# Kernel tuning notes

Hardware: AMD Instinct MI355X
Metric: run time of the kernel (lower is better)

The kernel has to match this reference:

```python
import jax, jax.numpy as jnp
import numpy as np

DIM = 1024
N_HEADS = 16
HEAD_DIM = DIM // N_HEADS


def setup_inputs() -> dict:
    key = jax.random.key(0)
    k_x, k_wqkv, k_bqkv, k_wp, k_bp = jax.random.split(key, 5)
    s = 1.0 / np.sqrt(DIM)
    return {
        "x": jax.random.normal(k_x, (2, 2048, DIM), dtype=jnp.float32),
        "w_qkv": jax.random.uniform(k_wqkv, (3 * DIM, DIM), minval=-s, maxval=s, dtype=jnp.float32),
        "b_qkv": jax.random.uniform(k_bqkv, (3 * DIM,), minval=-s, maxval=s, dtype=jnp.float32),
        "w_proj": jax.random.uniform(k_wp, (DIM, DIM), minval=-s, maxval=s, dtype=jnp.float32),
        "b_proj": jax.random.uniform(k_bp, (DIM,), minval=-s, maxval=s, dtype=jnp.float32),
    }


def reference(x, w_qkv, b_qkv, w_proj, b_proj):
    B, S, D = x.shape
    H, Hd = N_HEADS, HEAD_DIM
    scale = jnp.asarray(Hd, x.dtype) ** 0.5
    qkv = x @ w_qkv.T + b_qkv                      # [B, S, 3D]
    q, k, v = jnp.split(qkv, 3, axis=-1)
    # [B, S, D] -> [B, H, S, Hd]
    q = q.reshape(B, S, H, Hd).transpose(0, 2, 1, 3)
    k = k.reshape(B, S, H, Hd).transpose(0, 2, 1, 3)
    v = v.reshape(B, S, H, Hd).transpose(0, 2, 1, 3)
    attn = jnp.einsum("bhqd,bhkd->bhqk", q, k) / scale
    attn = jax.nn.softmax(attn, axis=-1)
    out = jnp.einsum("bhqk,bhkd->bhqd", attn, v)   # [B, H, S, Hd]
    out = out.transpose(0, 2, 1, 3).reshape(B, S, D)
    return out @ w_proj.T + b_proj
```

## Files before the change

kernel.cpp:

```cpp
#include <hip/hip_runtime.h>

typedef __bf16 bf16;
typedef __bf16 bf16x4 __attribute__((ext_vector_type(4)));
typedef __bf16 bf16x8 __attribute__((ext_vector_type(8)));
typedef float f32x4 __attribute__((ext_vector_type(4)));
typedef float f32x16 __attribute__((ext_vector_type(16)));

#define DIMD 1024
#define NHEAD 16
#define HDIM 64
#define BATCH 2
#define SEQ 2048
#define MTOT (BATCH*SEQ)

#define EXP2F(x) __builtin_amdgcn_exp2f(x)

#define OFF_VT (0ull)
#define OFF_OB (8ull<<20)

__device__ __forceinline__ bf16x8 cvt8(float4 a, float4 b) {
  bf16x8 r = { (bf16)a.x, (bf16)a.y, (bf16)a.z, (bf16)a.w,
               (bf16)b.x, (bf16)b.y, (bf16)b.z, (bf16)b.w };
  return r;
}

__global__ __launch_bounds__(256, 3) void gemm_qkv(
    const float* __restrict__ x, const float* __restrict__ W,
    const float* __restrict__ bias,
    bf16* __restrict__ Qb, bf16* __restrict__ Kb, bf16* __restrict__ Vt)
{
  __shared__ bf16 lA[2][128 * 32];
  __shared__ bf16 lB[2][128 * 32];
  const int tid = threadIdx.x;
  const int wave = tid >> 6, lane = tid & 63;
  const int l15 = lane & 15, quad = lane >> 4;
  const int wm = wave >> 1, wn = wave & 1;
  const int tm = blockIdx.y * 128, tn = blockIdx.x * 128;

  f32x4 acc[4][4] = {};

  const int srow = tid >> 1, shalf = (tid & 1) * 16;
  const float* ga = &x[(size_t)(tm + srow) * DIMD + shalf];
  const float* gb = &W[(size_t)(tn + srow) * DIMD + shalf];

  float4 av0 = ((const float4*)ga)[0], av1 = ((const float4*)ga)[1];
  float4 av2 = ((const float4*)ga)[2], av3 = ((const float4*)ga)[3];
  float4 bv0 = ((const float4*)gb)[0], bv1 = ((const float4*)gb)[1];
  float4 bv2 = ((const float4*)gb)[2], bv3 = ((const float4*)gb)[3];

  for (int kt = 0; kt < 32; kt++) {
    bf16* sA = lA[kt & 1];
    bf16* sB = lB[kt & 1];
    *(bf16x8*)&sA[srow * 32 + shalf]     = cvt8(av0, av1);
    *(bf16x8*)&sA[srow * 32 + shalf + 8] = cvt8(av2, av3);
    *(bf16x8*)&sB[srow * 32 + shalf]     = cvt8(bv0, bv1);
    *(bf16x8*)&sB[srow * 32 + shalf + 8] = cvt8(bv2, bv3);
    __syncthreads();

    const int kn = ((kt + 1) & 31) * 32;
    const float4* gan = (const float4*)(ga + kn);
    const float4* gbn = (const float4*)(gb + kn);
    av0 = gan[0]; av1 = gan[1]; av2 = gan[2]; av3 = gan[3];
    bv0 = gbn[0]; bv1 = gbn[1]; bv2 = gbn[2]; bv3 = gbn[3];

    bf16x8 af[4], bfr[4];
#pragma unroll
    for (int i = 0; i < 4; i++)
      af[i] = *(const bf16x8*)&sA[(wm * 64 + i * 16 + l15) * 32 + quad * 8];
#pragma unroll
    for (int i = 0; i < 4; i++)
      bfr[i] = *(const bf16x8*)&sB[(wn * 64 + i * 16 + l15) * 32 + quad * 8];
#pragma unroll
    for (int i = 0; i < 4; i++)
#pragma unroll
      for (int j = 0; j < 4; j++)
        acc[i][j] = __builtin_amdgcn_mfma_f32_16x16x32_bf16(af[i], bfr[j], acc[i][j], 0, 0, 0);
  }

  const int sel = tn >> 10;
#pragma unroll
  for (int j = 0; j < 4; j++) {
    const int n = tn + wn * 64 + j * 16 + l15;
    const float bv = bias[n];
    const int d = n & 1023, h = d >> 6, hd = d & 63;
#pragma unroll
    for (int i = 0; i < 4; i++) {
      const int mbase = tm + wm * 64 + i * 16 + quad * 4;
      const int b = mbase >> 11, s0 = mbase & 2047;
      const int bh = b * NHEAD + h;
      if (sel == 2) {
        bf16x4 vv = { (bf16)(acc[i][j][0] + bv), (bf16)(acc[i][j][1] + bv),
                      (bf16)(acc[i][j][2] + bv), (bf16)(acc[i][j][3] + bv) };
        *(bf16x4*)&Vt[((size_t)bh * HDIM + hd) * SEQ + s0] = vv;
      } else {
#pragma unroll
        for (int r = 0; r < 4; r++) {
          float v = acc[i][j][r] + bv;
          if (sel == 0)
            Qb[((size_t)bh * SEQ + s0 + r) * HDIM + hd] = (bf16)(v * 0.18033688f);
          else
            Kb[((size_t)bh * SEQ + s0 + r) * HDIM + hd] = (bf16)v;
        }
      }
    }
  }
}

__global__ __launch_bounds__(256, 2) void gemm_proj(
    const bf16* __restrict__ A, const float* __restrict__ W,
    const float* __restrict__ bias, float* __restrict__ out)
{
  __shared__ bf16 lA[2][64 * 32];
  __shared__ bf16 lB[2][128 * 32];
  const int tid = threadIdx.x;
  const int wave = tid >> 6, lane = tid & 63;
  const int l15 = lane & 15, quad = lane >> 4;
  const int tm = blockIdx.y * 64, tn = blockIdx.x * 128;

  f32x4 acc[4][2] = {};

  const int arow = tid >> 2, ach = (tid & 3) * 8;
  const int brow = tid >> 1, bhalf = (tid & 1) * 16;
  const bf16* ga = &A[(size_t)(tm + arow) * DIMD + ach];
  const float* gb = &W[(size_t)(tn + brow) * DIMD + bhalf];

  uint4 ar = *(const uint4*)ga;
  float4 bv0 = ((const float4*)gb)[0], bv1 = ((const float4*)gb)[1];
  float4 bv2 = ((const float4*)gb)[2], bv3 = ((const float4*)gb)[3];

  for (int kt = 0; kt < 32; kt++) {
    bf16* sA = lA[kt & 1];
    bf16* sB = lB[kt & 1];
    *(uint4*)&sA[arow * 32 + ach]        = ar;
    *(bf16x8*)&sB[brow * 32 + bhalf]     = cvt8(bv0, bv1);
    *(bf16x8*)&sB[brow * 32 + bhalf + 8] = cvt8(bv2, bv3);
    __syncthreads();

    const int kn = ((kt + 1) & 31) * 32;
    ar = *(const uint4*)(ga + kn);
    const float4* gbn = (const float4*)(gb + kn);
    bv0 = gbn[0]; bv1 = gbn[1]; bv2 = gbn[2]; bv3 = gbn[3];

    bf16x8 af[4], bfr[2];
#pragma unroll
    for (int i = 0; i < 4; i++)
      af[i] = *(const bf16x8*)&sA[(i * 16 + l15) * 32 + quad * 8];
#pragma unroll
    for (int j = 0; j < 2; j++)
      bfr[j] = *(const bf16x8*)&sB[(wave * 32 + j * 16 + l15) * 32 + quad * 8];
#pragma unroll
    for (int i = 0; i < 4; i++)
#pragma unroll
      for (int j = 0; j < 2; j++)
        acc[i][j] = __builtin_amdgcn_mfma_f32_16x16x32_bf16(af[i], bfr[j], acc[i][j], 0, 0, 0);
  }

#pragma unroll
  for (int j = 0; j < 2; j++) {
    const int n = tn + wave * 32 + j * 16 + l15;
    const float bv = bias[n];
#pragma unroll
    for (int i = 0; i < 4; i++) {
      const int mbase = tm + i * 16 + quad * 4;
#pragma unroll
      for (int r = 0; r < 4; r++)
        out[(size_t)(mbase + r) * DIMD + n] = acc[i][j][r] + bv;
    }
  }
}

#define LSTR 72
__global__ __launch_bounds__(256, 2) void attn_kernel(
    const bf16* __restrict__ Qb, const bf16* __restrict__ Kb,
    const bf16* __restrict__ Vt, bf16* __restrict__ Ob)
{
  __shared__ bf16 lKV[2][2][64 * LSTR];
  __shared__ bf16 lP[4][32 * LSTR];

  const int tid = threadIdx.x;
  const int wave = tid >> 6, lane = tid & 63;
  const int l31 = lane & 31, h = lane >> 5;
  const int xcd = blockIdx.x & 7, grp = blockIdx.x >> 3;
  const int bh = xcd + 8 * (grp & 3);
  const int qt = grp >> 2;

  const int qrow = qt * 128 + wave * 32 + l31;
  const bf16* qp = Qb + ((size_t)bh * SEQ + qrow) * HDIM + h * 8;
  bf16x8 qf[4];
#pragma unroll
  for (int c = 0; c < 4; c++) qf[c] = *(const bf16x8*)(qp + c * 16);

  const int srow = tid >> 3;
  const int sch = (tid & 7) * 8;
  const bf16* kg = Kb + ((size_t)bh * SEQ + srow) * HDIM + sch;
  const bf16* vg = Vt + ((size_t)bh * HDIM + srow) * SEQ + sch;

  uint4 kr0 = *(const uint4*)(kg);
  uint4 kr1 = *(const uint4*)(kg + 32 * HDIM);
  uint4 vr0 = *(const uint4*)(vg);
  uint4 vr1 = *(const uint4*)(vg + 32 * SEQ);

  f32x16 o0 = {}, o1 = {};
  float mrow = -1e30f, lrow = 0.f;

  for (int kt = 0; kt < SEQ / 64; kt++) {
    bf16* sK = lKV[kt & 1][0];
    bf16* sV = lKV[kt & 1][1];
    *(uint4*)&sK[srow * LSTR + sch]        = kr0;
    *(uint4*)&sK[(32 + srow) * LSTR + sch] = kr1;
    *(uint4*)&sV[srow * LSTR + sch]        = vr0;
    *(uint4*)&sV[(32 + srow) * LSTR + sch] = vr1;
    __syncthreads();

    const int ktn = (kt + 1) & (SEQ / 64 - 1);
    kr0 = *(const uint4*)(kg + (size_t)ktn * 64 * HDIM);
    kr1 = *(const uint4*)(kg + (size_t)ktn * 64 * HDIM + 32 * HDIM);
    vr0 = *(const uint4*)(vg + ktn * 64);
    vr1 = *(const uint4*)(vg + ktn * 64 + 32 * SEQ);

    f32x16 s0 = {}, s1 = {};
#pragma unroll
    for (int c = 0; c < 4; c++) {
      bf16x8 k0 = *(const bf16x8*)&sK[l31 * LSTR + c * 16 + h * 8];
      bf16x8 k1 = *(const bf16x8*)&sK[(32 + l31) * LSTR + c * 16 + h * 8];
      s0 = __builtin_amdgcn_mfma_f32_32x32x16_bf16(k0, qf[c], s0, 0, 0, 0);
      s1 = __builtin_amdgcn_mfma_f32_32x32x16_bf16(k1, qf[c], s1, 0, 0, 0);
    }

    float mx = -1e30f;
#pragma unroll
    for (int r = 0; r < 16; r++) { mx = fmaxf(mx, s0[r]); mx = fmaxf(mx, s1[r]); }
    mx = fmaxf(mx, __shfl_xor(mx, 32, 64));
    const float nm = fmaxf(mrow, mx);
    const float alpha = EXP2F(mrow - nm);
    mrow = nm;

    float rs = 0.f;
#pragma unroll
    for (int r = 0; r < 16; r++) {
      const float p0 = EXP2F(s0[r] - nm);
      const float p1 = EXP2F(s1[r] - nm);
      s0[r] = p0; s1[r] = p1;
      rs += p0 + p1;
    }
    rs += __shfl_xor(rs, 32, 64);
    lrow = lrow * alpha + rs;
#pragma unroll
    for (int r = 0; r < 16; r++) { o0[r] *= alpha; o1[r] *= alpha; }

#pragma unroll
    for (int g = 0; g < 4; g++) {
      bf16x4 pa = { (bf16)s0[4*g], (bf16)s0[4*g+1], (bf16)s0[4*g+2], (bf16)s0[4*g+3] };
      bf16x4 pb = { (bf16)s1[4*g], (bf16)s1[4*g+1], (bf16)s1[4*g+2], (bf16)s1[4*g+3] };
      *(bf16x4*)&lP[wave][l31 * LSTR + g * 8 + h * 4]      = pa;
      *(bf16x4*)&lP[wave][l31 * LSTR + 32 + g * 8 + h * 4] = pb;
    }
    bf16x8 pf[4];
#pragma unroll
    for (int c = 0; c < 4; c++)
      pf[c] = *(const bf16x8*)&lP[wave][l31 * LSTR + c * 16 + h * 8];

#pragma unroll
    for (int c = 0; c < 4; c++) {
      bf16x8 v0 = *(const bf16x8*)&sV[l31 * LSTR + c * 16 + h * 8];
      bf16x8 v1 = *(const bf16x8*)&sV[(32 + l31) * LSTR + c * 16 + h * 8];
      o0 = __builtin_amdgcn_mfma_f32_32x32x16_bf16(v0, pf[c], o0, 0, 0, 0);
      o1 = __builtin_amdgcn_mfma_f32_32x32x16_bf16(v1, pf[c], o1, 0, 0, 0);
    }
  }

  const int b = bh >> 4, head = bh & 15;
  const float inv = 1.f / lrow;
  const size_t base = ((size_t)b * SEQ + qrow) * DIMD + head * HDIM;
#pragma unroll
  for (int g = 0; g < 4; g++) {
    bf16x4 oa = { (bf16)(o0[4*g] * inv), (bf16)(o0[4*g+1] * inv),
                  (bf16)(o0[4*g+2] * inv), (bf16)(o0[4*g+3] * inv) };
    bf16x4 ob = { (bf16)(o1[4*g] * inv), (bf16)(o1[4*g+1] * inv),
                  (bf16)(o1[4*g+2] * inv), (bf16)(o1[4*g+3] * inv) };
    *(bf16x4*)&Ob[base + g * 8 + h * 4]      = oa;
    *(bf16x4*)&Ob[base + 32 + g * 8 + h * 4] = ob;
  }
}

extern "C" void kernel_launch(void* const* d_in, const int* in_sizes, int n_in,
                              void* d_out, int out_size, void* d_ws, size_t ws_size,
                              hipStream_t stream) {
  const float* x      = (const float*)d_in[0];
  const float* w_qkv  = (const float*)d_in[1];
  const float* b_qkv  = (const float*)d_in[2];
  const float* w_proj = (const float*)d_in[3];
  const float* b_proj = (const float*)d_in[4];
  float* out = (float*)d_out;
  char* ws = (char*)d_ws;

  bf16* Qb = (bf16*)d_out;
  bf16* Kb = (bf16*)d_out + (size_t)MTOT * DIMD;
  bf16* Vt = (bf16*)(ws + OFF_VT);
  bf16* Ob = (bf16*)(ws + OFF_OB);

  gemm_qkv<<<dim3(24, 32), 256, 0, stream>>>(x, w_qkv, b_qkv, Qb, Kb, Vt);
  attn_kernel<<<BATCH * NHEAD * (SEQ / 128), 256, 0, stream>>>(Qb, Kb, Vt, Ob);
  gemm_proj<<<dim3(8, 64), 256, 0, stream>>>(Ob, w_proj, b_proj, out);
}
```

Before: 216.7 us.

## Pre-convert x to bf16 and stream A tiles via global_load_lds

Adds a separate conversion kernel that writes x to bf16 in the workspace. The QKV GEMM then loads its A operand straight into LDS with global_load_lds instead of loading fp32 through registers and converting. The projection GEMM gets the same direct-to-LDS path for its bf16 A operand. The aim is to cut the A-side global traffic and register and conversion work, at the cost of an extra kernel launch and an extra pass over x. The workspace layout is shuffled so xb and Ob share offset 0.

Measured after the change: 209.4 us. 1.04x faster.

```diff
diff --git a/kernel.cpp b/kernel.cpp
--- a/kernel.cpp
+++ b/kernel.cpp
@@ -15,8 +15,16 @@
 
 #define EXP2F(x) __builtin_amdgcn_exp2f(x)
 
-#define OFF_VT (0ull)
-#define OFF_OB (8ull<<20)
+#define OFF_XB (0ull)
+#define OFF_OB (0ull)
+#define OFF_VT (8ull<<20)
+
+__device__ __forceinline__ void g2l16(const void* g, void* l) {
+  __builtin_amdgcn_global_load_lds(
+      (const __attribute__((address_space(1))) void*)g,
+      (__attribute__((address_space(3))) void*)l,
+      16, 0, 0);
+}
 
 __device__ __forceinline__ bf16x8 cvt8(float4 a, float4 b) {
   bf16x8 r = { (bf16)a.x, (bf16)a.y, (bf16)a.z, (bf16)a.w,
@@ -24,8 +32,18 @@
   return r;
 }
 
+__global__ __launch_bounds__(256) void cvt_kernel(const float* __restrict__ in,
+                                                  bf16* __restrict__ out, int n4) {
+  int i = blockIdx.x * blockDim.x + threadIdx.x;
+  if (i < n4) {
+    float4 v = ((const float4*)in)[i];
+    bf16x4 o = { (bf16)v.x, (bf16)v.y, (bf16)v.z, (bf16)v.w };
+    ((bf16x4*)out)[i] = o;
+  }
+}
+
 __global__ __launch_bounds__(256, 3) void gemm_qkv(
-    const float* __restrict__ x, const float* __restrict__ W,
+    const bf16* __restrict__ A, const float* __restrict__ W,
     const float* __restrict__ bias,
     bf16* __restrict__ Qb, bf16* __restrict__ Kb, bf16* __restrict__ Vt)
 {
@@ -39,30 +57,34 @@
 
   f32x4 acc[4][4] = {};
 
-  const int srow = tid >> 1, shalf = (tid & 1) * 16;
-  const float* ga = &x[(size_t)(tm + srow) * DIMD + shalf];
-  const float* gb = &W[(size_t)(tn + srow) * DIMD + shalf];
-
-  float4 av0 = ((const float4*)ga)[0], av1 = ((const float4*)ga)[1];
-  float4 av2 = ((const float4*)ga)[2], av3 = ((const float4*)ga)[3];
+  const int srow = tid >> 2, sch = (tid & 3) * 8;
+  const bf16*  ga = &A[(size_t)(tm + srow) * DIMD + sch];
+  const float* gb = &W[(size_t)(tn + srow) * DIMD + sch];
+
+  g2l16(ga,                     &lA[0][wave * 512]);
+  g2l16(ga + (size_t)64 * DIMD, &lA[0][2048 + wave * 512]);
   float4 bv0 = ((const float4*)gb)[0], bv1 = ((const float4*)gb)[1];
-  float4 bv2 = ((const float4*)gb)[2], bv3 = ((const float4*)gb)[3];
+  float4 bv2 = ((const float4*)(gb + (size_t)64 * DIMD))[0],
+         bv3 = ((const float4*)(gb + (size_t)64 * DIMD))[1];
 
   for (int kt = 0; kt < 32; kt++) {
-    bf16* sA = lA[kt & 1];
     bf16* sB = lB[kt & 1];
-    *(bf16x8*)&sA[srow * 32 + shalf]     = cvt8(av0, av1);
-    *(bf16x8*)&sA[srow * 32 + shalf + 8] = cvt8(av2, av3);
-    *(bf16x8*)&sB[srow * 32 + shalf]     = cvt8(bv0, bv1);
-    *(bf16x8*)&sB[srow * 32 + shalf + 8] = cvt8(bv2, bv3);
+    *(bf16x8*)&sB[srow * 32 + sch]        = cvt8(bv0, bv1);
+    *(bf16x8*)&sB[(64 + srow) * 32 + sch] = cvt8(bv2, bv3);
     __syncthreads();
 
-    const int kn = ((kt + 1) & 31) * 32;
-    const float4* gan = (const float4*)(ga + kn);
-    const float4* gbn = (const float4*)(gb + kn);
-    av0 = gan[0]; av1 = gan[1]; av2 = gan[2]; av3 = gan[3];
-    bv0 = gbn[0]; bv1 = gbn[1]; bv2 = gbn[2]; bv3 = gbn[3];
-
+    if (kt < 31) {
+      const int kn = (kt + 1) * 32;
+      bf16* nA = lA[(kt + 1) & 1];
+      g2l16(ga + kn,                     &nA[wave * 512]);
+      g2l16(ga + kn + (size_t)64 * DIMD, &nA[2048 + wave * 512]);
+      const float* gbn = gb + kn;
+      bv0 = ((const float4*)gbn)[0]; bv1 = ((const float4*)gbn)[1];
+      bv2 = ((const float4*)(gbn + (size_t)64 * DIMD))[0];
+      bv3 = ((const float4*)(gbn + (size_t)64 * DIMD))[1];
+    }
+
+    const bf16* sA = lA[kt & 1];
     bf16x8 af[4], bfr[4];
 #pragma unroll
     for (int i = 0; i < 4; i++)
@@ -119,28 +141,31 @@
 
   f32x4 acc[4][2] = {};
 
-  const int arow = tid >> 2, ach = (tid & 3) * 8;
-  const int brow = tid >> 1, bhalf = (tid & 1) * 16;
-  const bf16* ga = &A[(size_t)(tm + arow) * DIMD + ach];
-  const float* gb = &W[(size_t)(tn + brow) * DIMD + bhalf];
-
-  uint4 ar = *(const uint4*)ga;
+  const int srow = tid >> 2, sch = (tid & 3) * 8;
+  const bf16*  ga = &A[(size_t)(tm + srow) * DIMD + sch];
+  const float* gb = &W[(size_t)(tn + srow) * DIMD + sch];
+
+  g2l16(ga, &lA[0][wave * 512]);
   float4 bv0 = ((const float4*)gb)[0], bv1 = ((const float4*)gb)[1];
-  float4 bv2 = ((const float4*)gb)[2], bv3 = ((const float4*)gb)[3];
+  float4 bv2 = ((const float4*)(gb + (size_t)64 * DIMD))[0],
+         bv3 = ((const float4*)(gb + (size_t)64 * DIMD))[1];
 
   for (int kt = 0; kt < 32; kt++) {
-    bf16* sA = lA[kt & 1];
     bf16* sB = lB[kt & 1];
-    *(uint4*)&sA[arow * 32 + ach]        = ar;
-    *(bf16x8*)&sB[brow * 32 + bhalf]     = cvt8(bv0, bv1);
-    *(bf16x8*)&sB[brow * 32 + bhalf + 8] = cvt8(bv2, bv3);
+    *(bf16x8*)&sB[srow * 32 + sch]        = cvt8(bv0, bv1);
+    *(bf16x8*)&sB[(64 + srow) * 32 + sch] = cvt8(bv2, bv3);
     __syncthreads();
 
-    const int kn = ((kt + 1) & 31) * 32;
-    ar = *(const uint4*)(ga + kn);
-    const float4* gbn = (const float4*)(gb + kn);
-    bv0 = gbn[0]; bv1 = gbn[1]; bv2 = gbn[2]; bv3 = gbn[3];
-
+    if (kt < 31) {
+      const int kn = (kt + 1) * 32;
+      g2l16(ga + kn, &lA[(kt + 1) & 1][wave * 512]);
+      const float* gbn = gb + kn;
+      bv0 = ((const float4*)gbn)[0]; bv1 = ((const float4*)gbn)[1];
+      bv2 = ((const float4*)(gbn + (size_t)64 * DIMD))[0];
+      bv3 = ((const float4*)(gbn + (size_t)64 * DIMD))[1];
+    }
+
+    const bf16* sA = lA[kt & 1];
     bf16x8 af[4], bfr[2];
 #pragma unroll
     for (int i = 0; i < 4; i++)
@@ -296,10 +321,12 @@
 
   bf16* Qb = (bf16*)d_out;
   bf16* Kb = (bf16*)d_out + (size_t)MTOT * DIMD;
+  bf16* xb = (bf16*)(ws + OFF_XB);
+  bf16* Ob = (bf16*)(ws + OFF_OB);
   bf16* Vt = (bf16*)(ws + OFF_VT);
-  bf16* Ob = (bf16*)(ws + OFF_OB);
-
-  gemm_qkv<<<dim3(24, 32), 256, 0, stream>>>(x, w_qkv, b_qkv, Qb, Kb, Vt);
+
+  cvt_kernel<<<(MTOT * DIMD / 4) / 256, 256, 0, stream>>>(x, xb, MTOT * DIMD / 4);
+  gemm_qkv<<<dim3(24, 32), 256, 0, stream>>>(xb, w_qkv, b_qkv, Qb, Kb, Vt);
   attn_kernel<<<BATCH * NHEAD * (SEQ / 128), 256, 0, stream>>>(Qb, Kb, Vt, Ob);
   gemm_proj<<<dim3(8, 64), 256, 0, stream>>>(Ob, w_proj, b_proj, out);
 }
```
